# Optimization experiments

Hardware: AMD Instinct MI355X
Metric: run time of the kernel (lower is better)

The kernel has to match this reference:

```python
import jax, jax.numpy as jnp
import numpy as np

N_USERS = 50000
N_ITEMS = 20000
N_EDGES = 1_000_000
N_RATINGS = 5
IN_FEAT = 64
HID_FEAT = 64


def setup_inputs() -> dict:
    key = jax.random.key(0)
    k = jax.random.split(key, 6)
    u_s = jax.random.randint(k[0], (N_EDGES,), 0, N_USERS, dtype=jnp.int32)
    v_s = jax.random.randint(k[1], (N_EDGES,), 0, N_ITEMS, dtype=jnp.int32)
    rate = jax.random.randint(k[2], (N_EDGES,), 0, N_RATINGS, dtype=jnp.int32)
    x_user = jax.random.normal(k[3], (N_USERS, IN_FEAT), dtype=jnp.float32)
    x_item = jax.random.normal(k[4], (N_ITEMS, IN_FEAT), dtype=jnp.float32)
    # xavier-uniform with relu gain, as in nn.init.xavier_uniform_(gain=calculate_gain('relu'))
    gain = float(np.sqrt(2.0))
    bound = gain * float(np.sqrt(6.0 / (IN_FEAT + HID_FEAT)))
    weight = jax.random.uniform(k[5], (N_RATINGS, IN_FEAT, HID_FEAT),
                                minval=-bound, maxval=bound, dtype=jnp.float32)
    return {"u_s": u_s, "v_s": v_s, "rate": rate,
            "x_user": x_user, "x_item": x_item, "weight": weight}


def _aggregate(dst, src_feat, rate, n_dst, weight):
    # c_ij in the original = #edges sharing (dst node, rating); so the
    # sum over edges of (x[src] @ W[rate]) / c_ij equals a per-(dst, rating)
    # MEAN of source features followed by the rating-specific matmul.
    seg = dst * N_RATINGS + rate                      # [E] combined segment id
    cnt = jax.ops.segment_sum(jnp.ones_like(src_feat[:, 0]), seg,
                              num_segments=n_dst * N_RATINGS)  # [n_dst*R]
    ssum = jax.ops.segment_sum(src_feat, seg,
                               num_segments=n_dst * N_RATINGS)  # [n_dst*R, in]
    mean = ssum / jnp.maximum(cnt, 1.0)[:, None]
    mean = mean.reshape(n_dst, N_RATINGS, src_feat.shape[1])  # [n_dst, R, in]
    return jnp.einsum('nrd,rdh->nh', mean, weight)            # [n_dst, hid]


def reference(u_s, v_s, rate, x_user, x_item, weight):
    # w_sharing=False -> use weight directly; activation=None; dropout=0 -> identity
    h_u = _aggregate(u_s, x_item[v_s], rate, N_USERS, weight)
    h_v = _aggregate(v_s, x_user[u_s], rate, N_ITEMS, weight)
    return h_u, h_v
```

## Files before the change

### kernel.cpp

```cpp
#include <hip/hip_runtime.h>
#include <hip/hip_bf16.h>

constexpr int N_USERS = 50000;
constexpr int N_ITEMS = 20000;
constexpr int RATES   = 5;
constexpr int F       = 64;

constexpr int N_TOTAL  = N_USERS + N_ITEMS;
constexpr long OUT_FLOATS = (long)N_TOTAL * F;

constexpr int NFB_U = (N_USERS + 31) / 32;
constexpr int NFB_V = (N_ITEMS + 31) / 32;
constexpr int NFBK  = NFB_U + NFB_V;
constexpr int NBKP  = 2304;

constexpr int PBLK = 1024;
constexpr int EPT  = 8;
constexpr int EPB  = EPT * PBLK;

constexpr int SLOT = 2048;
constexpr int GCAP = SLOT;

constexpr int SMSTR = 328;

constexpr int LW_TOT = RATES * 8 * 512;

constexpr int TU8 = N_USERS * 8;
constexpr int TI8 = N_ITEMS * 8;
constexpr int TW8 = RATES * 8 * 64;
constexpr int TPREP = TU8 + TI8 + TW8;
constexpr int GPREP = (TPREP + PBLK - 1) / PBLK;

typedef short bfrag __attribute__((ext_vector_type(8)));
typedef float vf4   __attribute__((ext_vector_type(4)));

static __device__ __forceinline__ unsigned short f2bf(float f) {
    __hip_bfloat16 h = __float2bfloat16(f);
    return *reinterpret_cast<unsigned short*>(&h);
}

static __device__ __forceinline__ void accum8(float* acc, uint4 y) {
    unsigned uu[4] = {y.x, y.y, y.z, y.w};
#pragma unroll
    for (int qq = 0; qq < 4; qq++) {
        acc[2 * qq]     += __uint_as_float(uu[qq] << 16);
        acc[2 * qq + 1] += __uint_as_float(uu[qq] & 0xffff0000u);
    }
}

__global__ void zero_ints(int* __restrict__ p, long n) {
    long i = (long)blockIdx.x * blockDim.x + threadIdx.x;
    long stride = (long)gridDim.x * blockDim.x;
    for (long k = i; k < n; k += stride) p[k] = 0;
}

__global__ __launch_bounds__(PBLK) void fused_pp_kernel(
        const int* __restrict__ u_s, const int* __restrict__ v_s,
        const int* __restrict__ rate,
        const float* __restrict__ Xu, const float* __restrict__ Xi,
        const float* __restrict__ W,
        unsigned short* __restrict__ Xbu, unsigned short* __restrict__ Xbi,
        unsigned short* __restrict__ LWg,
        int* __restrict__ bcursor, int* __restrict__ sorted_pk,
        int n_edges, int npart) {
    __shared__ int sh[2 * NBKP];
    int tid = threadIdx.x;

    if ((int)blockIdx.x < npart) {
        int* lcnt = sh;
        int* lcur = sh + NBKP;
        int e0 = blockIdx.x * EPB;
        int eEnd = min(e0 + EPB, n_edges);
        int e = e0 + tid * EPT;
        bool full = (e + EPT <= eEnd);

        int uu[EPT], vv[EPT];
        int nv = 0;
        if (full) {
            int4 a = *(const int4*)(u_s + e);
            int4 b = *(const int4*)(u_s + e + 4);
            uu[0] = a.x; uu[1] = a.y; uu[2] = a.z; uu[3] = a.w;
            uu[4] = b.x; uu[5] = b.y; uu[6] = b.z; uu[7] = b.w;
            int4 c = *(const int4*)(v_s + e);
            int4 d = *(const int4*)(v_s + e + 4);
            vv[0] = c.x; vv[1] = c.y; vv[2] = c.z; vv[3] = c.w;
            vv[4] = d.x; vv[5] = d.y; vv[6] = d.z; vv[7] = d.w;
            nv = EPT;
        } else {
            for (int k = 0; e + k < eEnd; k++) {
                uu[k] = u_s[e + k];
                vv[k] = v_s[e + k];
                nv++;
            }
        }

        for (int i = tid; i < NBKP; i += PBLK) lcnt[i] = 0;
        __syncthreads();
        for (int k = 0; k < nv; k++) {
            atomicAdd(&lcnt[uu[k] >> 5], 1);
            atomicAdd(&lcnt[NFB_U + (vv[k] >> 5)], 1);
        }
        __syncthreads();
        for (int bb = tid; bb < NFBK; bb += PBLK) {
            int c = lcnt[bb];
            lcur[bb] = c ? atomicAdd(&bcursor[bb], c) : 0;
        }
        __syncthreads();
        int rr[EPT];
        if (full) {
            int4 a = *(const int4*)(rate + e);
            int4 b = *(const int4*)(rate + e + 4);
            rr[0] = a.x; rr[1] = a.y; rr[2] = a.z; rr[3] = a.w;
            rr[4] = b.x; rr[5] = b.y; rr[6] = b.z; rr[7] = b.w;
        } else {
            for (int k = 0; e + k < eEnd; k++) rr[k] = rate[e + k];
        }
        for (int k = 0; k < nv; k++) {
            int bu = uu[k] >> 5;
            int pu = atomicAdd(&lcur[bu], 1);
            if (pu < SLOT)
                sorted_pk[(long)bu * SLOT + pu] =
                    vv[k] | (rr[k] << 16) | ((uu[k] & 31) << 19);
            int bv = NFB_U + (vv[k] >> 5);
            int pv = atomicAdd(&lcur[bv], 1);
            if (pv < SLOT)
                sorted_pk[(long)bv * SLOT + pv] =
                    uu[k] | (rr[k] << 16) | ((vv[k] & 31) << 19);
        }
    } else {
        int t = ((int)blockIdx.x - npart) * PBLK + tid;
        if (t < TPREP) {
            if (t < TU8 + TI8) {
                const float* src;
                unsigned short* dst;
                if (t < TU8) { src = Xu + (long)t * 8;         dst = Xbu + (long)t * 8; }
                else         { src = Xi + (long)(t - TU8) * 8; dst = Xbi + (long)(t - TU8) * 8; }
                float4 a = *(const float4*)src;
                float4 b = *(const float4*)(src + 4);
                union { bfrag v; unsigned short s[8]; } o;
                o.s[0] = f2bf(a.x); o.s[1] = f2bf(a.y);
                o.s[2] = f2bf(a.z); o.s[3] = f2bf(a.w);
                o.s[4] = f2bf(b.x); o.s[5] = f2bf(b.y);
                o.s[6] = f2bf(b.z); o.s[7] = f2bf(b.w);
                *(bfrag*)dst = o.v;
            } else {
                int t2 = t - TU8 - TI8;
                int r   = t2 >> 9;
                int u   = t2 & 511;
                int kfq = u >> 6;
                int h   = u & 63;
                int kf  = kfq >> 2, q = kfq & 3;
                union { bfrag v; unsigned short s[8]; } o;
#pragma unroll
                for (int j = 0; j < 8; j++)
                    o.s[j] = f2bf(W[(r * 64 + kf * 32 + q * 8 + j) * 64 + h]);
                *(bfrag*)&LWg[(((r * 2 + kf) * 4 + q) * 64 + h) * 8] = o.v;
            }
        }
    }
}

__global__ __launch_bounds__(256, 6) void gather_mfma_kernel(
        const int* __restrict__ sorted_pk,
        const int* __restrict__ bcursor,
        const unsigned short* __restrict__ Xbu,
        const unsigned short* __restrict__ Xbi,
        const unsigned short* __restrict__ LWg,
        float* __restrict__ out) {
    __shared__ unsigned short perm[GCAP];
    __shared__ int lcnt[32 * RATES];
    __shared__ int lcur[32 * RATES];
    __shared__ float sinvc[32 * RATES];
    __shared__ int wsum[4];
    __shared__ unsigned short smean[32][SMSTR];

    int tid = threadIdx.x, lane = tid & 63, wid = tid >> 6;

    int b = blockIdx.x;
    const unsigned short* Xb;
    float* o;
    int fb, node0, n_nodes;
    if (b < NFB_V) {
        fb = NFB_U + b; node0 = b * 32; n_nodes = N_ITEMS;
        Xb = Xbu; o = out + (long)N_USERS * F;
    } else {
        fb = b - NFB_V; node0 = fb * 32; n_nodes = N_USERS;
        Xb = Xbi; o = out;
    }
    int nn = min(32, n_nodes - node0);
    int nseg = nn * RATES;

    int cnt = min(bcursor[fb], SLOT);
    const int* pkbase = sorted_pk + (long)fb * SLOT;

    int rpk[8];
#pragma unroll
    for (int kk = 0; kk < 8; kk++) {
        int j = kk * 256 + tid;
        rpk[kk] = (j < cnt) ? pkbase[j] : -1;
    }

    if (tid < nseg) lcnt[tid] = 0;
    __syncthreads();
#pragma unroll
    for (int kk = 0; kk < 8; kk++) {
        int pk = rpk[kk];
        if (pk >= 0)
            atomicAdd(&lcnt[((pk >> 19) & 31) * RATES + ((pk >> 16) & 7)], 1);
    }
    __syncthreads();

    int sv = (tid < nseg) ? lcnt[tid] : 0;
    int inc = sv;
#pragma unroll
    for (int off = 1; off < 64; off <<= 1) {
        int x = __shfl_up(inc, off, 64);
        if (lane >= off) inc += x;
    }
    if (lane == 63 && wid < 3) wsum[wid] = inc;
    __syncthreads();
    int prefix = ((wid >= 1) ? wsum[0] : 0) + ((wid >= 2) ? wsum[1] : 0);
    int excl = prefix + inc - sv;
    if (tid < nseg) {
        lcur[tid]  = excl;
        sinvc[tid] = 1.0f / fmaxf((float)sv, 1.0f);
    }
    __syncthreads();

#pragma unroll
    for (int kk = 0; kk < 8; kk++) {
        int pk = rpk[kk];
        if (pk >= 0) {
            int p = atomicAdd(&lcur[((pk >> 19) & 31) * RATES + ((pk >> 16) & 7)], 1);
            if (p < GCAP) perm[p] = (unsigned short)(pk & 0xFFFF);
        }
    }
    __syncthreads();

    int g = lane >> 3, ci = lane & 7;
    const unsigned short* xp = Xb + ci * 8;
    for (int oct = wid; oct * 8 < nseg; oct += 4) {
        int sg = oct * 8 + g;
        bool act = sg < nseg;
        int S = act ? ((sg == 0) ? 0 : min(lcur[sg - 1], GCAP)) : 0;
        int E = act ? min(lcur[sg], GCAP) : 0;
        float acc[8];
#pragma unroll
        for (int k = 0; k < 8; k++) acc[k] = 0.f;
        int t = S;
        for (; t + 8 <= E; t += 8) {
            int s[8];
#pragma unroll
            for (int k = 0; k < 8; k++) s[k] = perm[t + k];
            uint4 y[8];
#pragma unroll
            for (int k = 0; k < 8; k++)
                y[k] = *(const uint4*)(xp + (long)s[k] * F);
#pragma unroll
            for (int k = 0; k < 8; k++) accum8(acc, y[k]);
        }
        for (; t + 4 <= E; t += 4) {
            int s0 = perm[t], s1 = perm[t + 1];
            int s2 = perm[t + 2], s3 = perm[t + 3];
            uint4 y0 = *(const uint4*)(xp + (long)s0 * F);
            uint4 y1 = *(const uint4*)(xp + (long)s1 * F);
            uint4 y2 = *(const uint4*)(xp + (long)s2 * F);
            uint4 y3 = *(const uint4*)(xp + (long)s3 * F);
            accum8(acc, y0); accum8(acc, y1);
            accum8(acc, y2); accum8(acc, y3);
        }
        for (; t < E; t++) {
            int s0 = perm[t];
            accum8(acc, *(const uint4*)(xp + (long)s0 * F));
        }
        if (act) {
            float sc = sinvc[sg];
            int n = sg / RATES;
            int r = sg - n * RATES;
            union { bfrag v8; unsigned short us[8]; } mv;
#pragma unroll
            for (int k = 0; k < 8; k++) mv.us[k] = f2bf(acc[k] * sc);
            *(bfrag*)&smean[n][r * F + ci * 8] = mv.v8;
        }
    }
    __syncthreads();

    int m = lane & 15, q = lane >> 4;
    int tile = wid & 1, ht0 = wid >> 1;
    if (tile * 16 < nn) {
        const unsigned short* smrow = &smean[tile * 16 + m][0];
        vf4 acc0 = {0.f, 0.f, 0.f, 0.f};
        vf4 acc1 = {0.f, 0.f, 0.f, 0.f};
#pragma unroll
        for (int r = 0; r < RATES; r++) {
            bfrag a0 = *(const bfrag*)(smrow + r * F + q * 8);
            bfrag a1 = *(const bfrag*)(smrow + r * F + 32 + q * 8);
            {
                int h = ht0 * 16 + m;
                bfrag b0 = *(const bfrag*)(LWg + ((r * 2 + 0) * 4 + q) * 512 + h * 8);
                bfrag b1 = *(const bfrag*)(LWg + ((r * 2 + 1) * 4 + q) * 512 + h * 8);
                acc0 = __builtin_amdgcn_mfma_f32_16x16x32_bf16(a0, b0, acc0, 0, 0, 0);
                acc0 = __builtin_amdgcn_mfma_f32_16x16x32_bf16(a1, b1, acc0, 0, 0, 0);
            }
            {
                int h = (ht0 + 2) * 16 + m;
                bfrag b0 = *(const bfrag*)(LWg + ((r * 2 + 0) * 4 + q) * 512 + h * 8);
                bfrag b1 = *(const bfrag*)(LWg + ((r * 2 + 1) * 4 + q) * 512 + h * 8);
                acc1 = __builtin_amdgcn_mfma_f32_16x16x32_bf16(a0, b0, acc1, 0, 0, 0);
                acc1 = __builtin_amdgcn_mfma_f32_16x16x32_bf16(a1, b1, acc1, 0, 0, 0);
            }
        }
        float* obase = o + (long)(node0 + tile * 16 + q * 4) * F;
#pragma unroll
        for (int reg = 0; reg < 4; reg++) {
            obase[(long)reg * F + ht0 * 16 + m]       = acc0[reg];
            obase[(long)reg * F + (ht0 + 2) * 16 + m] = acc1[reg];
        }
    }
}

extern "C" void kernel_launch(void* const* d_in, const int* in_sizes, int n_in,
                              void* d_out, int out_size, void* d_ws, size_t ws_size,
                              hipStream_t stream) {
    const int*   u_s    = (const int*)d_in[0];
    const int*   v_s    = (const int*)d_in[1];
    const int*   rate   = (const int*)d_in[2];
    const float* x_user = (const float*)d_in[3];
    const float* x_item = (const float*)d_in[4];
    const float* W      = (const float*)d_in[5];
    float* out = (float*)d_out;

    int n_edges = in_sizes[0];
    int npart = (n_edges + EPB - 1) / EPB;

    unsigned short* Xbu = (unsigned short*)d_ws;
    unsigned short* Xbi = Xbu + (long)N_USERS * F;
    unsigned short* LWg = Xbi + (long)N_ITEMS * F;
    int* bcursor      = (int*)(LWg + LW_TOT);
    int* sorted_pk    = bcursor + NFBK;
    size_t need = (size_t)((char*)(sorted_pk + (long)NFBK * SLOT) - (char*)d_ws);
    if (need > ws_size) {
        zero_ints<<<2048, 256, 0, stream>>>((int*)out, OUT_FLOATS);
        return;
    }

    zero_ints<<<1, 256, 0, stream>>>(bcursor, NFBK);

    fused_pp_kernel<<<npart + GPREP, PBLK, 0, stream>>>(
        u_s, v_s, rate, x_user, x_item, W,
        Xbu, Xbi, LWg, bcursor, sorted_pk, n_edges, npart);

    gather_mfma_kernel<<<NFBK, 256, 0, stream>>>(
        sorted_pk, bcursor, Xbu, Xbi, LWg, out);
}
```

Before: 143.9 us.

## Shrink node buckets to 16 per block with per-side slot capacities

Halves the bucket width from 32 to 16 destination nodes, doubling the number of gather blocks. Slot capacity is now per side: 512 for user buckets and 1024 for item buckets. Edges per partition thread drop to 4, and the MFMA stage uses one 16-row tile per block, with each wave computing a 16-column slice. The aim is more parallelism, less LDS per block and higher occupancy (launch bounds 7); tail handling is dropped because node counts divide by 16. The smaller slot capacities raise the risk of overflowing edges being silently truncated on skewed degree distributions.

```diff
diff --git a/kernel.cpp b/kernel.cpp
--- a/kernel.cpp
+++ b/kernel.cpp
@@ -9,17 +9,19 @@
 constexpr int N_TOTAL  = N_USERS + N_ITEMS;
 constexpr long OUT_FLOATS = (long)N_TOTAL * F;
 
-constexpr int NFB_U = (N_USERS + 31) / 32;
-constexpr int NFB_V = (N_ITEMS + 31) / 32;
+constexpr int NFB_U = N_USERS / 16;
+constexpr int NFB_V = N_ITEMS / 16;
 constexpr int NFBK  = NFB_U + NFB_V;
-constexpr int NBKP  = 2304;
+constexpr int NBKP  = 4608;
 
 constexpr int PBLK = 1024;
-constexpr int EPT  = 8;
+constexpr int EPT  = 4;
 constexpr int EPB  = EPT * PBLK;
 
-constexpr int SLOT = 2048;
-constexpr int GCAP = SLOT;
+constexpr int SLOT_U = 512;
+constexpr int SLOT_V = 1024;
+constexpr long VOFF  = (long)NFB_U * SLOT_U;
+constexpr int PCAP   = 1024;
 
 constexpr int SMSTR = 328;
 
@@ -78,13 +80,9 @@
         int nv = 0;
         if (full) {
             int4 a = *(const int4*)(u_s + e);
-            int4 b = *(const int4*)(u_s + e + 4);
             uu[0] = a.x; uu[1] = a.y; uu[2] = a.z; uu[3] = a.w;
-            uu[4] = b.x; uu[5] = b.y; uu[6] = b.z; uu[7] = b.w;
             int4 c = *(const int4*)(v_s + e);
-            int4 d = *(const int4*)(v_s + e + 4);
             vv[0] = c.x; vv[1] = c.y; vv[2] = c.z; vv[3] = c.w;
-            vv[4] = d.x; vv[5] = d.y; vv[6] = d.z; vv[7] = d.w;
             nv = EPT;
         } else {
             for (int k = 0; e + k < eEnd; k++) {
@@ -97,8 +95,8 @@
         for (int i = tid; i < NBKP; i += PBLK) lcnt[i] = 0;
         __syncthreads();
         for (int k = 0; k < nv; k++) {
-            atomicAdd(&lcnt[uu[k] >> 5], 1);
-            atomicAdd(&lcnt[NFB_U + (vv[k] >> 5)], 1);
+            atomicAdd(&lcnt[uu[k] >> 4], 1);
+            atomicAdd(&lcnt[NFB_U + (vv[k] >> 4)], 1);
         }
         __syncthreads();
         for (int bb = tid; bb < NFBK; bb += PBLK) {
@@ -109,23 +107,21 @@
         int rr[EPT];
         if (full) {
             int4 a = *(const int4*)(rate + e);
-            int4 b = *(const int4*)(rate + e + 4);
             rr[0] = a.x; rr[1] = a.y; rr[2] = a.z; rr[3] = a.w;
-            rr[4] = b.x; rr[5] = b.y; rr[6] = b.z; rr[7] = b.w;
         } else {
             for (int k = 0; e + k < eEnd; k++) rr[k] = rate[e + k];
         }
         for (int k = 0; k < nv; k++) {
-            int bu = uu[k] >> 5;
+            int bu = uu[k] >> 4;
             int pu = atomicAdd(&lcur[bu], 1);
-            if (pu < SLOT)
-                sorted_pk[(long)bu * SLOT + pu] =
-                    vv[k] | (rr[k] << 16) | ((uu[k] & 31) << 19);
-            int bv = NFB_U + (vv[k] >> 5);
-            int pv = atomicAdd(&lcur[bv], 1);
-            if (pv < SLOT)
-                sorted_pk[(long)bv * SLOT + pv] =
-                    uu[k] | (rr[k] << 16) | ((vv[k] & 31) << 19);
+            if (pu < SLOT_U)
+                sorted_pk[(long)bu * SLOT_U + pu] =
+                    vv[k] | (rr[k] << 16) | ((uu[k] & 15) << 19);
+            int bv = vv[k] >> 4;
+            int pv = atomicAdd(&lcur[NFB_U + bv], 1);
+            if (pv < SLOT_V)
+                sorted_pk[VOFF + (long)bv * SLOT_V + pv] =
+                    uu[k] | (rr[k] << 16) | ((vv[k] & 15) << 19);
         }
     } else {
         int t = ((int)blockIdx.x - npart) * PBLK + tid;
@@ -160,42 +156,45 @@
     }
 }
 
-__global__ __launch_bounds__(256, 6) void gather_mfma_kernel(
+__global__ __launch_bounds__(256, 7) void gather_mfma_kernel(
         const int* __restrict__ sorted_pk,
         const int* __restrict__ bcursor,
         const unsigned short* __restrict__ Xbu,
         const unsigned short* __restrict__ Xbi,
         const unsigned short* __restrict__ LWg,
         float* __restrict__ out) {
-    __shared__ unsigned short perm[GCAP];
-    __shared__ int lcnt[32 * RATES];
-    __shared__ int lcur[32 * RATES];
-    __shared__ float sinvc[32 * RATES];
+    __shared__ unsigned short perm[PCAP];
+    __shared__ int lcnt[16 * RATES];
+    __shared__ int lcur[16 * RATES];
+    __shared__ float sinvc[16 * RATES];
     __shared__ int wsum[4];
-    __shared__ unsigned short smean[32][SMSTR];
+    __shared__ unsigned short smean[16][SMSTR];
 
     int tid = threadIdx.x, lane = tid & 63, wid = tid >> 6;
 
     int b = blockIdx.x;
     const unsigned short* Xb;
     float* o;
-    int fb, node0, n_nodes;
+    const int* pkbase;
+    int fb, node0;
     if (b < NFB_V) {
-        fb = NFB_U + b; node0 = b * 32; n_nodes = N_ITEMS;
+        fb = NFB_U + b; node0 = b * 16;
         Xb = Xbu; o = out + (long)N_USERS * F;
+        pkbase = sorted_pk + VOFF + (long)b * SLOT_V;
     } else {
-        fb = b - NFB_V; node0 = fb * 32; n_nodes = N_USERS;
+        int ub = b - NFB_V;
+        fb = ub; node0 = ub * 16;
         Xb = Xbi; o = out;
-    }
-    int nn = min(32, n_nodes - node0);
-    int nseg = nn * RATES;
-
-    int cnt = min(bcursor[fb], SLOT);
-    const int* pkbase = sorted_pk + (long)fb * SLOT;
-
-    int rpk[8];
-#pragma unroll
-    for (int kk = 0; kk < 8; kk++) {
+        pkbase = sorted_pk + (long)ub * SLOT_U;
+    }
+    constexpr int nseg = 16 * RATES;
+
+    int cap = (b < NFB_V) ? SLOT_V : SLOT_U;
+    int cnt = min(bcursor[fb], cap);
+
+    int rpk[4];
+#pragma unroll
+    for (int kk = 0; kk < 4; kk++) {
         int j = kk * 256 + tid;
         rpk[kk] = (j < cnt) ? pkbase[j] : -1;
     }
@@ -203,10 +202,10 @@
     if (tid < nseg) lcnt[tid] = 0;
     __syncthreads();
 #pragma unroll
-    for (int kk = 0; kk < 8; kk++) {
+    for (int kk = 0; kk < 4; kk++) {
         int pk = rpk[kk];
         if (pk >= 0)
-            atomicAdd(&lcnt[((pk >> 19) & 31) * RATES + ((pk >> 16) & 7)], 1);
+            atomicAdd(&lcnt[((pk >> 19) & 15) * RATES + ((pk >> 16) & 7)], 1);
     }
     __syncthreads();
 
@@ -228,11 +227,11 @@
     __syncthreads();
 
 #pragma unroll
-    for (int kk = 0; kk < 8; kk++) {
+    for (int kk = 0; kk < 4; kk++) {
         int pk = rpk[kk];
         if (pk >= 0) {
-            int p = atomicAdd(&lcur[((pk >> 19) & 31) * RATES + ((pk >> 16) & 7)], 1);
-            if (p < GCAP) perm[p] = (unsigned short)(pk & 0xFFFF);
+            int p = atomicAdd(&lcur[((pk >> 19) & 15) * RATES + ((pk >> 16) & 7)], 1);
+            if (p < PCAP) perm[p] = (unsigned short)(pk & 0xFFFF);
         }
     }
     __syncthreads();
@@ -241,9 +240,8 @@
     const unsigned short* xp = Xb + ci * 8;
     for (int oct = wid; oct * 8 < nseg; oct += 4) {
         int sg = oct * 8 + g;
-        bool act = sg < nseg;
-        int S = act ? ((sg == 0) ? 0 : min(lcur[sg - 1], GCAP)) : 0;
-        int E = act ? min(lcur[sg], GCAP) : 0;
+        int S = (sg == 0) ? 0 : min(lcur[sg - 1], PCAP);
+        int E = min(lcur[sg], PCAP);
         float acc[8];
 #pragma unroll
         for (int k = 0; k < 8; k++) acc[k] = 0.f;
@@ -273,7 +271,7 @@
             int s0 = perm[t];
             accum8(acc, *(const uint4*)(xp + (long)s0 * F));
         }
-        if (act) {
+        {
             float sc = sinvc[sg];
             int n = sg / RATES;
             int r = sg - n * RATES;
@@ -286,36 +284,23 @@
     __syncthreads();
 
     int m = lane & 15, q = lane >> 4;
-    int tile = wid & 1, ht0 = wid >> 1;
-    if (tile * 16 < nn) {
-        const unsigned short* smrow = &smean[tile * 16 + m][0];
-        vf4 acc0 = {0.f, 0.f, 0.f, 0.f};
-        vf4 acc1 = {0.f, 0.f, 0.f, 0.f};
+    {
+        const unsigned short* smrow = &smean[m][0];
+        vf4 acc = {0.f, 0.f, 0.f, 0.f};
+        int h = wid * 16 + m;
 #pragma unroll
         for (int r = 0; r < RATES; r++) {
             bfrag a0 = *(const bfrag*)(smrow + r * F + q * 8);
             bfrag a1 = *(const bfrag*)(smrow + r * F + 32 + q * 8);
-            {
-                int h = ht0 * 16 + m;
-                bfrag b0 = *(const bfrag*)(LWg + ((r * 2 + 0) * 4 + q) * 512 + h * 8);
-                bfrag b1 = *(const bfrag*)(LWg + ((r * 2 + 1) * 4 + q) * 512 + h * 8);
-                acc0 = __builtin_amdgcn_mfma_f32_16x16x32_bf16(a0, b0, acc0, 0, 0, 0);
-                acc0 = __builtin_amdgcn_mfma_f32_16x16x32_bf16(a1, b1, acc0, 0, 0, 0);
-            }
-            {
-                int h = (ht0 + 2) * 16 + m;
-                bfrag b0 = *(const bfrag*)(LWg + ((r * 2 + 0) * 4 + q) * 512 + h * 8);
-                bfrag b1 = *(const bfrag*)(LWg + ((r * 2 + 1) * 4 + q) * 512 + h * 8);
-                acc1 = __builtin_amdgcn_mfma_f32_16x16x32_bf16(a0, b0, acc1, 0, 0, 0);
-                acc1 = __builtin_amdgcn_mfma_f32_16x16x32_bf16(a1, b1, acc1, 0, 0, 0);
-            }
-        }
-        float* obase = o + (long)(node0 + tile * 16 + q * 4) * F;
-#pragma unroll
-        for (int reg = 0; reg < 4; reg++) {
-            obase[(long)reg * F + ht0 * 16 + m]       = acc0[reg];
-            obase[(long)reg * F + (ht0 + 2) * 16 + m] = acc1[reg];
-        }
+            bfrag b0 = *(const bfrag*)(LWg + ((r * 2 + 0) * 4 + q) * 512 + h * 8);
+            bfrag b1 = *(const bfrag*)(LWg + ((r * 2 + 1) * 4 + q) * 512 + h * 8);
+            acc = __builtin_amdgcn_mfma_f32_16x16x32_bf16(a0, b0, acc, 0, 0, 0);
+            acc = __builtin_amdgcn_mfma_f32_16x16x32_bf16(a1, b1, acc, 0, 0, 0);
+        }
+        float* obase = o + (long)(node0 + q * 4) * F;
+#pragma unroll
+        for (int reg = 0; reg < 4; reg++)
+            obase[(long)reg * F + wid * 16 + m] = acc[reg];
     }
 }
 
@@ -338,7 +323,8 @@
     unsigned short* LWg = Xbi + (long)N_ITEMS * F;
     int* bcursor      = (int*)(LWg + LW_TOT);
     int* sorted_pk    = bcursor + NFBK;
-    size_t need = (size_t)((char*)(sorted_pk + (long)NFBK * SLOT) - (char*)d_ws);
+    long pk_ints = VOFF + (long)NFB_V * SLOT_V;
+    size_t need = (size_t)((char*)(sorted_pk + pk_ints) - (char*)d_ws);
     if (need > ws_size) {
         zero_ints<<<2048, 256, 0, stream>>>((int*)out, OUT_FLOATS);
         return;
```

Measured after the change: 158.7 us. 10.2% more time.
